# Kernel optimization log

Measured on AMD Instinct MI355X. Metric: run time of the kernel, lower is better.

The kernel has to match this reference:

```python
import jax, jax.numpy as jnp
import numpy as np

B, T, C, HEAD = 4, 4096, 2048, 128
ROPE_BASE = 10000.0


def _rope_tables(T, dim):
    # precompute_freqs_cis: freqs = 1/base^(2i/dim), angles = t * freqs
    inv_freq = 1.0 / (ROPE_BASE ** (np.arange(0, dim, 2, dtype=np.float32) / dim))
    angles = np.arange(T, dtype=np.float32)[:, None] * inv_freq[None, :]  # [T, dim/2]
    return jnp.asarray(np.cos(angles)), jnp.asarray(np.sin(angles))


def _apply_rope(x, cos, sin):
    # x: [B, T, D]; interleaved complex pairs (x[2i], x[2i+1]) rotated by angle
    B_, T_, D = x.shape
    xr = x.reshape(B_, T_, D // 2, 2)
    x1, x2 = xr[..., 0], xr[..., 1]
    o1 = x1 * cos - x2 * sin
    o2 = x1 * sin + x2 * cos
    return jnp.stack([o1, o2], axis=-1).reshape(B_, T_, D)


def setup_inputs() -> dict:
    key0 = jax.random.key(0)
    k1, k2, k3, k4 = jax.random.split(key0, 4)
    x = jax.random.normal(k1, (B, T, C), dtype=jnp.float32)
    key = jax.random.normal(k2, (B, T, HEAD), dtype=jnp.float32)
    value = jax.random.normal(k3, (B, T, HEAD), dtype=jnp.float32)
    w_q = jax.random.normal(k4, (HEAD, C), dtype=jnp.float32) * 0.02
    return {"x": x, "key": key, "value": value, "w_q": w_q}


def reference(x, key, value, w_q):
    # query projection (nn.Linear, no bias)
    q = jnp.einsum('btc,dc->btd', x, w_q)  # [B, T, HEAD]
    cos, sin = _rope_tables(T, HEAD)
    # apply_rotary_emb(key, query) returns (key_rot, query_rot); then
    # query, key = (key_rot, query_rot) and wei = key @ query^T == q_rot @ k_rot^T
    q_rot = _apply_rope(q, cos, sin)
    k_rot = _apply_rope(key, cos, sin)
    scale = HEAD ** -0.5
    wei = jnp.einsum('btd,bsd->bts', q_rot, k_rot) * scale  # [B, T, T]
    causal = jnp.tril(jnp.ones((T, T), dtype=bool))
    wei = jnp.where(causal, wei, -jnp.inf)
    wei = jax.nn.softmax(wei, axis=-1)
    # dropout is identity in eval / p=0
    return jnp.einsum('bts,bsd->btd', wei, value)  # [B, T, HEAD]
```

## Files before the change

### kernel.cpp

```cpp
#include <hip/hip_runtime.h>
#include <hip/hip_bf16.h>

#define TSEQ  4096
#define NBATCH 4
#define CDIM  2048
#define DH    128

typedef __bf16 bf16x8 __attribute__((ext_vector_type(8)));
typedef float  f32x4  __attribute__((ext_vector_type(4)));
typedef unsigned short u16x8 __attribute__((ext_vector_type(8)));
typedef unsigned       u32x4 __attribute__((ext_vector_type(4)));
typedef unsigned short u16;

__device__ __forceinline__ u16 f2bf(float f) {
  union { float f; unsigned u; } v; v.f = f;
  unsigned r = (v.u + 0x7FFFu + ((v.u >> 16) & 1u)) >> 16;
  return (u16)r;
}
__device__ __forceinline__ float bf2f(u16 h) {
  union { unsigned u; float f; } v; v.u = ((unsigned)h) << 16;
  return v.f;
}
__device__ __forceinline__ bf16x8 ld_bf8(const u16* p) {
  return __builtin_bit_cast(bf16x8, *(const u16x8*)p);
}
__device__ __forceinline__ unsigned pk2(float lo, float hi) {
  float2 f; f.x = lo; f.y = hi;
  __hip_bfloat162 h = __float22bfloat162_rn(f);
  unsigned r; __builtin_memcpy(&r, &h, 4);
  return r;
}
__device__ __forceinline__ u16x8 cvt8u(float4 a, float4 b) {
  u32x4 u;
  u[0] = pk2(a.x, a.y); u[1] = pk2(a.z, a.w);
  u[2] = pk2(b.x, b.y); u[3] = pk2(b.z, b.w);
  return __builtin_bit_cast(u16x8, u);
}

__device__ __forceinline__ void lds_barrier() {
  asm volatile("s_waitcnt lgkmcnt(0)" ::: "memory");
  __builtin_amdgcn_s_barrier();
}

template<int CTRL>
__device__ __forceinline__ float dppmv(float x) {
  return __builtin_bit_cast(float,
    __builtin_amdgcn_update_dpp(0, __builtin_bit_cast(int, x), CTRL, 0xF, 0xF, true));
}
__device__ __forceinline__ float red_max16(float v) {
  v = fmaxf(v, dppmv<0xB1>(v));
  v = fmaxf(v, dppmv<0x4E>(v));
  v = fmaxf(v, dppmv<0x124>(v));
  v = fmaxf(v, dppmv<0x128>(v));
  return v;
}
__device__ __forceinline__ float red_sum16(float v) {
  v += dppmv<0xB1>(v);
  v += dppmv<0x4E>(v);
  v += dppmv<0x124>(v);
  v += dppmv<0x128>(v);
  return v;
}

__device__ __forceinline__ int unit_base(int Q) {
  int a = Q >> 2, bq = Q & 3;
  return 2 * a * (a + 1) + bq * (a + 1);
}

__global__ __launch_bounds__(256) void k_prep(const float* __restrict__ w, u16* __restrict__ wbf,
                                              const float* __restrict__ key, u16* __restrict__ krot,
                                              const float* __restrict__ value, u16* __restrict__ vt) {
  __shared__ u16 S[128 * 66];
  int bid = blockIdx.x;
  int tid = threadIdx.x;

  if (bid < 256) {
    int b = bid >> 6;
    int t0 = (bid & 63) * 64;
    int d = (tid & 31) * 4;
    int tl0 = tid >> 5;
#pragma unroll
    for (int i = 0; i < 8; ++i) {
      int tl = tl0 + i * 8;
      const float4 val = *(const float4*)(value + ((size_t)(b * TSEQ + t0 + tl)) * DH + d);
      S[(d + 0) * 66 + tl] = f2bf(val.x);
      S[(d + 1) * 66 + tl] = f2bf(val.y);
      S[(d + 2) * 66 + tl] = f2bf(val.z);
      S[(d + 3) * 66 + tl] = f2bf(val.w);
    }
    __syncthreads();
#pragma unroll
    for (int i = 0; i < 16; ++i) {
      int idx = tid + i * 256;
      int dd = idx >> 5;
      int tw = (idx & 31) * 2;
      unsigned lo = S[dd * 66 + tw];
      unsigned hi = S[dd * 66 + tw + 1];
      *(unsigned*)(vt + ((size_t)(b * DH + dd)) * TSEQ + t0 + tw) = lo | (hi << 16);
    }
    return;
  }

  if (bid < 512) {
    int i = (bid - 256) * 256 + tid;
    const float4 v = *(const float4*)(w + (size_t)i * 4);
    uint2 o; o.x = pk2(v.x, v.y); o.y = pk2(v.z, v.w);
    *(uint2*)(wbf + (size_t)i * 4) = o;
    return;
  }

  int idx = (bid - 512) * 256 + tid;
  int f0 = idx * 4;
  int row = f0 >> 7;
  int d = f0 & 127;
  int p = d >> 1;
  int t = row & (TSEQ - 1);
  const float4 kv = *(const float4*)(key + (size_t)row * DH + d);
  float inv0 = powf(10000.0f, -(float)p / 64.0f);
  float inv1 = powf(10000.0f, -(float)(p + 1) / 64.0f);
  float s0, c0, s1, c1;
  sincosf((float)t * inv0, &s0, &c0);
  sincosf((float)t * inv1, &s1, &c1);
  uint2 o;
  o.x = pk2(kv.x * c0 - kv.y * s0, kv.x * s0 + kv.y * c0);
  o.y = pk2(kv.z * c1 - kv.w * s1, kv.z * s1 + kv.w * c1);
  *(uint2*)(krot + (size_t)row * DH + d) = o;
}

__global__ __launch_bounds__(512, 4) void k_qproj(const float* __restrict__ x,
                                                  const u16* __restrict__ wbf,
                                                  u16* __restrict__ qrot) {
  __shared__ u16 Al[16 * 32 * 8];
  int bid = blockIdx.x;
  int tid = threadIdx.x;
  int w = tid >> 6;
  int lane = tid & 63;
  int l15 = lane & 15;
  int quad = lane >> 4;
  int m0 = bid * 32;
  int dcol = w * 16 + l15;

  int srow = tid >> 4;
  int chunk = tid & 15;
  int prow = (srow + chunk) & 31;
  const float* xg = x + (size_t)(m0 + srow) * CDIM + chunk * 8;
  const u16* wp = wbf + (size_t)dcol * CDIM + quad * 8;

  f32x4 acc[2];
  acc[0] = (f32x4){0.f, 0.f, 0.f, 0.f};
  acc[1] = (f32x4){0.f, 0.f, 0.f, 0.f};

  float4 paA[2], paB[2];
  paA[0] = *(const float4*)(xg);       paA[1] = *(const float4*)(xg + 4);
  paB[0] = *(const float4*)(xg + 128); paB[1] = *(const float4*)(xg + 132);

  auto qstep = [&](float4 (&pa)[2], int itc) {
    u16x8 st = cvt8u(pa[0], pa[1]);
    if (itc + 2 < CDIM / 128) {
      const float* xn = xg + (size_t)(itc + 2) * 128;
      pa[0] = *(const float4*)xn;
      pa[1] = *(const float4*)(xn + 4);
    }
    lds_barrier();
    *(u16x8*)&Al[(chunk * 32 + prow) * 8] = st;
    lds_barrier();
    int k0 = itc * 128;
#pragma unroll
    for (int ks = 0; ks < 4; ++ks) {
      int ch = ks * 4 + quad;
      bf16x8 bfrag = ld_bf8(wp + k0 + ks * 32);
#pragma unroll
      for (int mt = 0; mt < 2; ++mt) {
        int rr = (mt * 16 + l15 + ch) & 31;
        bf16x8 af = ld_bf8(&Al[(ch * 32 + rr) * 8]);
        acc[mt] = __builtin_amdgcn_mfma_f32_16x16x32_bf16(af, bfrag, acc[mt], 0, 0, 0);
      }
    }
  };

#pragma unroll 1
  for (int ith = 0; ith < 8; ++ith) {
    qstep(paA, 2 * ith);
    qstep(paB, 2 * ith + 1);
  }

  const float scale = 0.08838834764831845f;
  int p = dcol >> 1;
  float inv = powf(10000.0f, -(float)p / 64.0f);
#pragma unroll
  for (int mt = 0; mt < 2; ++mt) {
#pragma unroll
    for (int r = 0; r < 4; ++r) {
      int m = m0 + mt * 16 + quad * 4 + r;
      int t = m & (TSEQ - 1);
      float ang = (float)t * inv;
      float s, c; sincosf(ang, &s, &c);
      float val = acc[mt][r];
      float partner = __shfl_xor(val, 1, 64);
      float o = (lane & 1) ? (val * c + partner * s) : (val * c - partner * s);
      qrot[(size_t)m * DH + dcol] = f2bf(o * scale);
    }
  }
}

__global__ __launch_bounds__(256, 2) void k_attn(const u16* __restrict__ qrot,
                                                 const u16* __restrict__ krot,
                                                 const u16* __restrict__ vt,
                                                 u16* __restrict__ Opart,
                                                 float2* __restrict__ ml) {
  __shared__ u16 Kl[16 * 64 * 8];
  __shared__ u16 Vl[8 * 128 * 8];
  __shared__ u16 Pl[4 * 32 * 72];

  int bid = blockIdx.x;
  int b = bid / 144;
  int u = 143 - (bid - b * 144);
  int uid = b * 144 + u;
  int Q = 0;
#pragma unroll 1
  for (int q = 31; q >= 0; --q) {
    if (unit_base(q) <= u) { Q = q; break; }
  }
  int kc = u - unit_base(Q);
  int nkt = 2 * Q + 2;
  int kt0 = kc * 8;
  int kt1 = min(kt0 + 8, nkt);
  int m0 = Q * 128;

  int tid = threadIdx.x;
  int w = tid >> 6;
  int lane = tid & 63;
  int l15 = lane & 15;
  int quad = lane >> 4;
  u16* pw = Pl + w * 32 * 72;

  int rK = tid & 63;   int jgK = tid >> 6;
  int dV = tid & 127;  int hV = tid >> 7;

  const u16* kb = krot + (size_t)b * TSEQ * DH;
  const u16* vb = vt + (size_t)b * DH * TSEQ;

  bf16x8 qf[2][4];
#pragma unroll
  for (int mt = 0; mt < 2; ++mt) {
    const u16* qb = qrot + ((size_t)(b * TSEQ + m0 + mt * 64 + w * 16 + l15)) * DH + quad * 8;
#pragma unroll
    for (int c = 0; c < 4; ++c) qf[mt][c] = ld_bf8(qb + c * 32);
  }

  f32x4 o_acc[2][8];
#pragma unroll
  for (int mt = 0; mt < 2; ++mt)
#pragma unroll
    for (int i = 0; i < 8; ++i) o_acc[mt][i] = (f32x4){0.f, 0.f, 0.f, 0.f};
  float m_st[2][4], l_st[2][4];
#pragma unroll
  for (int mt = 0; mt < 2; ++mt)
#pragma unroll
    for (int r = 0; r < 4; ++r) { m_st[mt][r] = -INFINITY; l_st[mt][r] = 0.f; }

  u16x8 kr[4], vr[4];
  {
    const u16* ks = kb + (size_t)(kt0 * 64 + rK) * DH + jgK * 32;
    const u16* vs = vb + (size_t)dV * TSEQ + kt0 * 64 + hV * 32;
#pragma unroll
    for (int i = 0; i < 4; ++i) { kr[i] = *(const u16x8*)(ks + i * 8); vr[i] = *(const u16x8*)(vs + i * 8); }
  }

  for (int kt = kt0; kt < kt1; ++kt) {
    lds_barrier();
#pragma unroll
    for (int i = 0; i < 4; ++i) {
      *(u16x8*)&Kl[((jgK * 4 + i) * 64 + rK) * 8] = kr[i];
      *(u16x8*)&Vl[((hV * 4 + i) * 128 + dV) * 8] = vr[i];
    }
    lds_barrier();
    if (kt + 1 < kt1) {
      const u16* ks = kb + (size_t)((kt + 1) * 64 + rK) * DH + jgK * 32;
      const u16* vs = vb + (size_t)dV * TSEQ + (kt + 1) * 64 + hV * 32;
#pragma unroll
      for (int i = 0; i < 4; ++i) { kr[i] = *(const u16x8*)(ks + i * 8); vr[i] = *(const u16x8*)(vs + i * 8); }
    }

    f32x4 s[2][4];
#pragma unroll
    for (int mt = 0; mt < 2; ++mt)
#pragma unroll
      for (int nt = 0; nt < 4; ++nt) s[mt][nt] = (f32x4){0.f, 0.f, 0.f, 0.f};
    __builtin_amdgcn_s_setprio(1);
#pragma unroll
    for (int c = 0; c < 4; ++c)
#pragma unroll
      for (int nt = 0; nt < 4; ++nt) {
        bf16x8 kf = ld_bf8(&Kl[((c * 4 + quad) * 64 + nt * 16 + l15) * 8]);
#pragma unroll
        for (int mt = 0; mt < 2; ++mt)
          s[mt][nt] = __builtin_amdgcn_mfma_f32_16x16x32_bf16(qf[mt][c], kf, s[mt][nt], 0, 0, 0);
      }
    __builtin_amdgcn_s_setprio(0);

    if (kt * 64 >= m0) {
#pragma unroll
      for (int mt = 0; mt < 2; ++mt)
#pragma unroll
        for (int nt = 0; nt < 4; ++nt)
#pragma unroll
          for (int r = 0; r < 4; ++r) {
            int key_g = kt * 64 + nt * 16 + l15;
            int row_g = m0 + mt * 64 + w * 16 + quad * 4 + r;
            if (key_g > row_g) s[mt][nt][r] = -INFINITY;
          }
    }

    float alpha[2][4];
    int chg = 0;
#pragma unroll
    for (int mt = 0; mt < 2; ++mt)
#pragma unroll
      for (int r = 0; r < 4; ++r) {
        float rm = fmaxf(fmaxf(s[mt][0][r], s[mt][1][r]), fmaxf(s[mt][2][r], s[mt][3][r]));
        rm = red_max16(rm);
        float mn = fmaxf(m_st[mt][r], rm);
        float al = __expf(m_st[mt][r] - mn);
        m_st[mt][r] = mn;
        float ps = 0.f;
#pragma unroll
        for (int nt = 0; nt < 4; ++nt) {
          float pv = __expf(s[mt][nt][r] - mn);
          s[mt][nt][r] = pv;
          ps += pv;
        }
        ps = red_sum16(ps);
        l_st[mt][r] = l_st[mt][r] * al + ps;
        alpha[mt][r] = al;
        chg |= (al != 1.0f);
      }
    if (__any(chg)) {
#pragma unroll
      for (int mt = 0; mt < 2; ++mt)
#pragma unroll
        for (int nt = 0; nt < 8; ++nt)
#pragma unroll
          for (int r = 0; r < 4; ++r) o_acc[mt][nt][r] *= alpha[mt][r];
    }

#pragma unroll
    for (int mt = 0; mt < 2; ++mt)
#pragma unroll
      for (int nt = 0; nt < 4; ++nt)
#pragma unroll
        for (int r = 0; r < 4; ++r)
          pw[(mt * 16 + quad * 4 + r) * 72 + nt * 16 + l15] = f2bf(s[mt][nt][r]);

#pragma unroll
    for (int c2 = 0; c2 < 2; ++c2) {
      bf16x8 pf[2];
#pragma unroll
      for (int mt = 0; mt < 2; ++mt)
        pf[mt] = ld_bf8(pw + (mt * 16 + l15) * 72 + c2 * 32 + quad * 8);
      __builtin_amdgcn_s_setprio(1);
#pragma unroll
      for (int nt = 0; nt < 8; ++nt) {
        bf16x8 vf = ld_bf8(&Vl[((c2 * 4 + quad) * 128 + nt * 16 + l15) * 8]);
#pragma unroll
        for (int mt = 0; mt < 2; ++mt)
          o_acc[mt][nt] = __builtin_amdgcn_mfma_f32_16x16x32_bf16(pf[mt], vf, o_acc[mt][nt], 0, 0, 0);
      }
      __builtin_amdgcn_s_setprio(0);
    }
  }

  u16* op = Opart + (size_t)uid * (128 * 128);
#pragma unroll
  for (int mt = 0; mt < 2; ++mt)
#pragma unroll
    for (int nt = 0; nt < 8; ++nt)
#pragma unroll
      for (int r = 0; r < 4; ++r)
        op[(mt * 64 + w * 16 + quad * 4 + r) * 128 + nt * 16 + l15] = f2bf(o_acc[mt][nt][r]);
  if (l15 == 0) {
#pragma unroll
    for (int mt = 0; mt < 2; ++mt)
#pragma unroll
      for (int r = 0; r < 4; ++r) {
        float2 p; p.x = m_st[mt][r]; p.y = l_st[mt][r];
        ml[(size_t)uid * 128 + mt * 64 + w * 16 + quad * 4 + r] = p;
      }
  }
}

__global__ __launch_bounds__(256) void k_merge(const u16* __restrict__ Opart,
                                               const float2* __restrict__ ml,
                                               float* __restrict__ out) {
  __shared__ float wgt[8][128];
  __shared__ float invL[128];
  int bid = blockIdx.x;
  int b = bid >> 5, Q = bid & 31;
  int C = (Q >> 2) + 1;
  int base = b * 144 + unit_base(Q);
  int tid = threadIdx.x;
  if (tid < 128) {
    float mv[8], lv[8];
    float M = -INFINITY;
    for (int c = 0; c < C; ++c) {
      float2 p = ml[(size_t)(base + c) * 128 + tid];
      mv[c] = p.x; lv[c] = p.y;
      M = fmaxf(M, p.x);
    }
    float L = 0.f;
    for (int c = 0; c < C; ++c) {
      float wv = __expf(mv[c] - M);
      wgt[c][tid] = wv;
      L += wv * lv[c];
    }
    invL[tid] = 1.f / L;
  }
  __syncthreads();
#pragma unroll
  for (int k = 0; k < 8; ++k) {
    int slot = tid + k * 256;
    int row = slot >> 4;
    float acc[8];
#pragma unroll
    for (int j = 0; j < 8; ++j) acc[j] = 0.f;
    for (int c = 0; c < C; ++c) {
      u16x8 v = *(const u16x8*)&Opart[(size_t)(base + c) * (128 * 128) + slot * 8];
      float wv = wgt[c][row];
#pragma unroll
      for (int j = 0; j < 8; ++j) acc[j] += wv * bf2f(v[j]);
    }
    float il = invL[row];
    float4 o0, o1;
    o0.x = acc[0] * il; o0.y = acc[1] * il; o0.z = acc[2] * il; o0.w = acc[3] * il;
    o1.x = acc[4] * il; o1.y = acc[5] * il; o1.z = acc[6] * il; o1.w = acc[7] * il;
    float* op = out + ((size_t)(b * TSEQ + Q * 128 + row)) * DH + (slot & 15) * 8;
    *(float4*)op = o0;
    *(float4*)(op + 4) = o1;
  }
}

extern "C" void kernel_launch(void* const* d_in, const int* in_sizes, int n_in,
                              void* d_out, int out_size, void* d_ws, size_t ws_size,
                              hipStream_t stream) {
  const float* x     = (const float*)d_in[0];
  const float* key   = (const float*)d_in[1];
  const float* value = (const float*)d_in[2];
  const float* w_q   = (const float*)d_in[3];
  float* out = (float*)d_out;

  char* ws = (char*)d_ws;
  u16* qrot   = (u16*)(ws);
  u16* krot   = (u16*)(ws + (4u  << 20));
  u16* vt     = (u16*)(ws + (8u  << 20));
  u16* Opart  = (u16*)(ws + (12u << 20));
  float2* ml  = (float2*)(ws + (31u << 20));
  u16* wbf    = (u16*)(ws + (32u << 20));

  k_prep<<<2560, 256, 0, stream>>>(w_q, wbf, key, krot, value, vt);
  k_qproj<<<(NBATCH * TSEQ) / 32, 512, 0, stream>>>(x, wbf, qrot);
  k_attn<<<NBATCH * 144, 256, 0, stream>>>(qrot, krot, vt, Opart, ml);
  k_merge<<<NBATCH * 32, 256, 0, stream>>>(Opart, ml, out);
}
```

Measured before the change: 292.8 us.

## Stage x tiles via direct global-to-LDS loads with double buffering in q projection

The query projection kernel no longer loads x into registers, converts it to bf16 and writes it to LDS. It now uses global_load_lds to copy fp32 rows of x straight into a double-buffered, XOR-swizzled LDS tile, and converts to bf16 only when building the MFMA fragments. Weight fragments for the next K-step are prefetched into registers during the current step. The aim is to cut register traffic and one barrier per step and to overlap the next tile's load with the current MFMAs. In exchange, LDS use grows fourfold and the fp32-to-bf16 conversion work now happens on every fragment read.

```diff
diff --git a/kernel.cpp b/kernel.cpp
--- a/kernel.cpp
+++ b/kernel.cpp
@@ -35,6 +35,12 @@
   u[0] = pk2(a.x, a.y); u[1] = pk2(a.z, a.w);
   u[2] = pk2(b.x, b.y); u[3] = pk2(b.z, b.w);
   return __builtin_bit_cast(u16x8, u);
+}
+
+__device__ __forceinline__ void gload16(const void* g, void* l) {
+  __builtin_amdgcn_global_load_lds(
+      (const __attribute__((address_space(1))) unsigned*)g,
+      (__attribute__((address_space(3))) unsigned*)l, 16, 0, 0);
 }
 
 __device__ __forceinline__ void lds_barrier() {
@@ -130,7 +136,7 @@
 __global__ __launch_bounds__(512, 4) void k_qproj(const float* __restrict__ x,
                                                   const u16* __restrict__ wbf,
                                                   u16* __restrict__ qrot) {
-  __shared__ u16 Al[16 * 32 * 8];
+  __shared__ float Al[2][32 * 128];
   int bid = blockIdx.x;
   int tid = threadIdx.x;
   int w = tid >> 6;
@@ -140,48 +146,53 @@
   int m0 = bid * 32;
   int dcol = w * 16 + l15;
 
-  int srow = tid >> 4;
-  int chunk = tid & 15;
-  int prow = (srow + chunk) & 31;
-  const float* xg = x + (size_t)(m0 + srow) * CDIM + chunk * 8;
+  int rA = 4 * w + (lane >> 5);
+  int rB = rA + 2;
+  const char* gA = (const char*)(x + (size_t)(m0 + rA) * CDIM) + (((lane & 31) * 16) ^ ((rA & 7) << 4));
+  const char* gB = (const char*)(x + (size_t)(m0 + rB) * CDIM) + (((lane & 31) * 16) ^ ((rB & 7) << 4));
+  char* lA0 = (char*)&Al[0][0] + (4 * w) * 512;
+  char* lB0 = lA0 + 1024;
+
   const u16* wp = wbf + (size_t)dcol * CDIM + quad * 8;
 
   f32x4 acc[2];
   acc[0] = (f32x4){0.f, 0.f, 0.f, 0.f};
   acc[1] = (f32x4){0.f, 0.f, 0.f, 0.f};
 
-  float4 paA[2], paB[2];
-  paA[0] = *(const float4*)(xg);       paA[1] = *(const float4*)(xg + 4);
-  paB[0] = *(const float4*)(xg + 128); paB[1] = *(const float4*)(xg + 132);
-
-  auto qstep = [&](float4 (&pa)[2], int itc) {
-    u16x8 st = cvt8u(pa[0], pa[1]);
-    if (itc + 2 < CDIM / 128) {
-      const float* xn = xg + (size_t)(itc + 2) * 128;
-      pa[0] = *(const float4*)xn;
-      pa[1] = *(const float4*)(xn + 4);
-    }
-    lds_barrier();
-    *(u16x8*)&Al[(chunk * 32 + prow) * 8] = st;
-    lds_barrier();
-    int k0 = itc * 128;
+  gload16(gA, lA0);
+  gload16(gB, lB0);
+  bf16x8 bfr[4];
+#pragma unroll
+  for (int ks = 0; ks < 4; ++ks) bfr[ks] = ld_bf8(wp + ks * 32);
+  __syncthreads();
+
+#pragma unroll 1
+  for (int it = 0; it < CDIM / 128; ++it) {
+    if (it + 1 < CDIM / 128) {
+      int nb = (it + 1) & 1;
+      gload16(gA + (size_t)(it + 1) * 512, lA0 + nb * 16384);
+      gload16(gB + (size_t)(it + 1) * 512, lB0 + nb * 16384);
+    }
+
+    const char* tile = (const char*)&Al[0][0] + (it & 1) * 16384;
 #pragma unroll
     for (int ks = 0; ks < 4; ++ks) {
-      int ch = ks * 4 + quad;
-      bf16x8 bfrag = ld_bf8(wp + k0 + ks * 32);
+      int cbase = ks * 128 + quad * 32;
 #pragma unroll
       for (int mt = 0; mt < 2; ++mt) {
-        int rr = (mt * 16 + l15 + ch) & 31;
-        bf16x8 af = ld_bf8(&Al[(ch * 32 + rr) * 8]);
-        acc[mt] = __builtin_amdgcn_mfma_f32_16x16x32_bf16(af, bfrag, acc[mt], 0, 0, 0);
+        int row = mt * 16 + l15;
+        int xr = (row & 7) << 4;
+        float4 f0 = *(const float4*)(tile + row * 512 + (cbase ^ xr));
+        float4 f1 = *(const float4*)(tile + row * 512 + ((cbase + 16) ^ xr));
+        bf16x8 af = __builtin_bit_cast(bf16x8, cvt8u(f0, f1));
+        acc[mt] = __builtin_amdgcn_mfma_f32_16x16x32_bf16(af, bfr[ks], acc[mt], 0, 0, 0);
       }
     }
-  };
-
-#pragma unroll 1
-  for (int ith = 0; ith < 8; ++ith) {
-    qstep(paA, 2 * ith);
-    qstep(paB, 2 * ith + 1);
+    if (it + 1 < CDIM / 128) {
+#pragma unroll
+      for (int ks = 0; ks < 4; ++ks) bfr[ks] = ld_bf8(wp + (it + 1) * 128 + ks * 32);
+    }
+    __syncthreads();
   }
 
   const float scale = 0.08838834764831845f;
```

New measurement: 284.7 us. 1.03x faster.
